# Performance work log

Measured on AMD Instinct MI355X. Metric: run time of the kernel, lower is better.

Reference implementation:

```python
import jax, jax.numpy as jnp
import numpy as np

ROPE_BASE = 10000.0

def _rope(x):
    # x: (B, S, D); canonical interleaved RoPE over sequence positions
    B, S, D = x.shape
    half = D // 2
    inv_freq = 1.0 / (ROPE_BASE ** (jnp.arange(half, dtype=x.dtype) * 2.0 / D))  # (half,)
    ang = jnp.arange(S, dtype=x.dtype)[:, None] * inv_freq[None, :]              # (S, half)
    cos, sin = jnp.cos(ang), jnp.sin(ang)
    x1 = x[..., 0::2]   # (B, S, half)
    x2 = x[..., 1::2]
    rot = jnp.stack([x1 * cos - x2 * sin, x1 * sin + x2 * cos], axis=-1)         # (B,S,half,2)
    return rot.reshape(B, S, D)

def setup_inputs() -> dict:
    key = jax.random.key(0)
    ks = jax.random.split(key, 7)
    B, S, D = 32, 1024, 768
    sc = 1.0 / np.sqrt(D)
    return {
        "x":  jax.random.normal(ks[0], (B, S, D), dtype=jnp.float32),
        "Wq": jax.random.normal(ks[1], (D, D), dtype=jnp.float32) * sc,
        "bq": jax.random.normal(ks[2], (D,), dtype=jnp.float32) * 0.01,
        "Wk": jax.random.normal(ks[3], (D, D), dtype=jnp.float32) * sc,
        "bk": jax.random.normal(ks[4], (D,), dtype=jnp.float32) * 0.01,
        "Wv": jax.random.normal(ks[5], (D, D), dtype=jnp.float32) * sc,
        "bv": jax.random.normal(ks[6], (D,), dtype=jnp.float32) * 0.01,
    }

def reference(x, Wq, bq, Wk, bk, Wv, bv):
    D = x.shape[-1]
    # torch nn.Linear: y = x @ W.T + b
    Q = jnp.einsum('bsd,ed->bse', x, Wq) + bq
    K = jnp.einsum('bsd,ed->bse', x, Wk) + bk
    V = jnp.einsum('bsd,ed->bse', x, Wv) + bv
    Q = _rope(Q)
    K = _rope(K)
    scores = jnp.einsum('bqd,bkd->bqk', Q, K) / jnp.sqrt(jnp.asarray(D, x.dtype))
    weights = jax.nn.softmax(scores, axis=-1)
    return jnp.einsum('bqk,bkd->bqd', weights, V)
```

## Files before the change

### kernel.cpp

```cpp
#include <hip/hip_runtime.h>


typedef __attribute__((ext_vector_type(8))) _Float16 f16x8;
typedef __attribute__((ext_vector_type(4))) float    f32x4;

__device__ __forceinline__ unsigned short f2h(float f) {
    _Float16 h = (_Float16)f;
    return __builtin_bit_cast(unsigned short, h);
}
__device__ __forceinline__ float h2f(unsigned short u) {
    return (float)__builtin_bit_cast(_Float16, u);
}

__device__ __forceinline__ void async_ld16(const void* g, void* l) {
    __builtin_amdgcn_global_load_lds(
        (const __attribute__((address_space(1))) void*)g,
        (__attribute__((address_space(3))) void*)l, 16, 0, 0);
}

template<int MODE, int KDIM, int LDA, int LDB>
__global__ __launch_bounds__(512, 2)
void gemm_bt(const unsigned short* __restrict__ A,
             const unsigned short* __restrict__ B,
             void* __restrict__ C0, void* __restrict__ C1,
             const float* __restrict__ bias0,
             const float* __restrict__ bias1,
             float scale)
{
    __shared__ __align__(16) unsigned short sA[2][256 * 64];
    __shared__ __align__(16) unsigned short sB[2][256 * 64];

    const int tid  = threadIdx.x;
    const int lane = tid & 63;
    const int wave = tid >> 6;
    const int wm   = wave >> 2;
    const int wn   = wave & 3;
    const int wrow = wm * 128;
    const int wcol = wn * 64;
    const int quad = lane >> 4;
    const int l15  = lane & 15;

    const int xcd = blockIdx.x & 7;
    const int bi  = blockIdx.x >> 3;
    int m0, n0, z = 0;
    if constexpr (MODE == 0) {
        m0 = (xcd * 16 + bi / 6) * 256;  n0 = (bi % 6) * 256;
    } else if constexpr (MODE == 1) {
        n0 = (xcd * 16 + bi / 3) * 256;  m0 = (bi % 3) * 256;
    } else if constexpr (MODE == 2) {
        z = xcd * 4 + bi / 16; const int t = bi % 16;
        m0 = (t >> 2) * 256; n0 = (t & 3) * 256;
    } else {
        z = xcd * 4 + bi / 12; const int t = bi % 12;
        m0 = (t / 3) * 256;  n0 = (t % 3) * 256;
    }

    const unsigned short* Ab = A;
    const unsigned short* Bb = B;
    if constexpr (MODE == 2) { Ab += (size_t)z * 786432;  Bb += (size_t)z * 786432; }
    if constexpr (MODE == 3) { Ab += (size_t)z * 1048576; Bb += (size_t)z * 786432; }

    const int srow = tid >> 3;
    const int sk   = ((tid & 7) ^ (srow & 7)) * 8;
    const int sdst = (tid & 7) * 8;

    auto stgA = [&](int buf, int r0, int kt) {
        async_ld16(Ab + (size_t)(m0 + r0 + srow) * LDA + kt + sk,
                   &sA[buf][(r0 + srow) * 64 + sdst]);
    };
    auto stgB = [&](int buf, int r0, int kt) {
        async_ld16(Bb + (size_t)(n0 + r0 + srow) * LDB + kt + sk,
                   &sB[buf][(r0 + srow) * 64 + sdst]);
    };

    f32x4 acc[8][4] = {};

    constexpr int NT = KDIM / 64;

    stgA(0, 0, 0); stgA(0, 128, 0); stgB(0, 0, 0); stgB(0, 64, 0);
    stgA(0, 64, 0); stgA(0, 192, 0); stgB(0, 128, 0); stgB(0, 192, 0);
    stgA(1, 0, 64); stgA(1, 128, 64); stgB(1, 0, 64); stgB(1, 64, 64);
    stgA(1, 64, 64); stgA(1, 192, 64); stgB(1, 128, 64); stgB(1, 192, 64);
    asm volatile("s_waitcnt vmcnt(8)" ::: "memory");
    __builtin_amdgcn_s_barrier();

    int p = 0;
    #pragma unroll 2
    for (int t = 0; t < NT; ++t, p ^= 1) {
        const int  kt2  = (t + 2) * 64;
        const bool pref = (t + 2) < NT;
        const unsigned short* sAp = sA[p];
        const unsigned short* sBp = sB[p];

        f16x8 bfr[4][2], af[4][2];
        #pragma unroll
        for (int ni = 0; ni < 4; ++ni) {
            const int r = wcol + ni * 16 + l15;
            const int x = r & 7;
            bfr[ni][0] = *(const f16x8*)&sBp[r * 64 + ((quad       ^ x) << 3)];
            bfr[ni][1] = *(const f16x8*)&sBp[r * 64 + (((4 + quad) ^ x) << 3)];
        }
        #pragma unroll
        for (int mi = 0; mi < 4; ++mi) {
            const int r = wrow + mi * 16 + l15;
            const int x = r & 7;
            af[mi][0] = *(const f16x8*)&sAp[r * 64 + ((quad       ^ x) << 3)];
            af[mi][1] = *(const f16x8*)&sAp[r * 64 + (((4 + quad) ^ x) << 3)];
        }
        asm volatile("s_waitcnt lgkmcnt(0)" ::: "memory");
        __builtin_amdgcn_s_barrier();
        if (pref) { stgA(p, 0, kt2); stgA(p, 128, kt2);
                    stgB(p, 0, kt2); stgB(p, 64, kt2); }
        __builtin_amdgcn_s_setprio(1);
        #pragma unroll
        for (int mi = 0; mi < 4; ++mi)
            #pragma unroll
            for (int ni = 0; ni < 4; ++ni) {
                acc[mi][ni] = __builtin_amdgcn_mfma_f32_16x16x32_f16(
                    af[mi][0], bfr[ni][0], acc[mi][ni], 0, 0, 0);
                acc[mi][ni] = __builtin_amdgcn_mfma_f32_16x16x32_f16(
                    af[mi][1], bfr[ni][1], acc[mi][ni], 0, 0, 0);
            }
        __builtin_amdgcn_s_setprio(0);

        #pragma unroll
        for (int mi = 0; mi < 4; ++mi) {
            const int r = wrow + 64 + mi * 16 + l15;
            const int x = r & 7;
            af[mi][0] = *(const f16x8*)&sAp[r * 64 + ((quad       ^ x) << 3)];
            af[mi][1] = *(const f16x8*)&sAp[r * 64 + (((4 + quad) ^ x) << 3)];
        }
        asm volatile("s_waitcnt lgkmcnt(0)" ::: "memory");
        __builtin_amdgcn_s_barrier();
        if (pref) { stgA(p, 64, kt2); stgA(p, 192, kt2);
                    stgB(p, 128, kt2); stgB(p, 192, kt2); }
        __builtin_amdgcn_s_setprio(1);
        #pragma unroll
        for (int mi = 0; mi < 4; ++mi)
            #pragma unroll
            for (int ni = 0; ni < 4; ++ni) {
                acc[4 + mi][ni] = __builtin_amdgcn_mfma_f32_16x16x32_f16(
                    af[mi][0], bfr[ni][0], acc[4 + mi][ni], 0, 0, 0);
                acc[4 + mi][ni] = __builtin_amdgcn_mfma_f32_16x16x32_f16(
                    af[mi][1], bfr[ni][1], acc[4 + mi][ni], 0, 0, 0);
            }
        __builtin_amdgcn_s_setprio(0);

        if (pref) asm volatile("s_waitcnt vmcnt(8)" ::: "memory");
        else      asm volatile("s_waitcnt vmcnt(0)" ::: "memory");
        __builtin_amdgcn_s_barrier();
    }

    const bool evenlane = (l15 & 1) == 0;

    float invf[4];
    if constexpr (MODE == 0) {
        #pragma unroll
        for (int ni = 0; ni < 4; ++ni) {
            int col = n0 + wcol + ni * 16 + l15;
            if (col >= 768) col -= 768;
            invf[ni] = exp2f((float)(col >> 1) * -0.03460341765507773f);
        }
    }

    #pragma unroll
    for (int mi = 0; mi < 8; ++mi) {
        const int rowoff = (mi & 3) * 16 + (mi >> 2) * 64;
        #pragma unroll
        for (int ni = 0; ni < 4; ++ni) {
            #pragma unroll
            for (int reg = 0; reg < 4; ++reg) {
                const int grow = m0 + wrow + rowoff + quad * 4 + reg;
                const int gcol = n0 + wcol + ni * 16 + l15;
                float v = acc[mi][ni][reg];
                if constexpr (MODE == 0) {
                    const bool isQ = gcol < 768;
                    const int  col = isQ ? gcol : gcol - 768;
                    v += isQ ? bias0[col] : bias1[col];
                    const float other = __shfl_xor(v, 1);
                    const int   s     = grow & 1023;
                    const float ang   = (float)s * invf[ni];
                    float sn, cs;
                    __sincosf(ang, &sn, &cs);
                    float r = (col & 1) ? fmaf(other, sn, v * cs)
                                        : fmaf(v, cs, -(other * sn));
                    if (isQ) r *= scale;
                    const unsigned short h = f2h(r);
                    const unsigned int packed =
                        (unsigned int)h | (__shfl_xor((unsigned int)h, 1) << 16);
                    if (evenlane) {
                        unsigned short* dst = (unsigned short*)(isQ ? C0 : C1);
                        *(unsigned int*)(dst + (size_t)grow * 768 + col) = packed;
                    }
                } else if constexpr (MODE == 1) {
                    v += bias0[grow];
                    const unsigned short h = f2h(v);
                    const unsigned int packed =
                        (unsigned int)h | (__shfl_xor((unsigned int)h, 1) << 16);
                    if (evenlane) {
                        const int b = gcol >> 10, s = gcol & 1023;
                        *(unsigned int*)((unsigned short*)C0 + (size_t)b * (768 * 1024)
                                         + (size_t)grow * 1024 + s) = packed;
                    }
                } else if constexpr (MODE == 2) {
                    const unsigned short h = f2h(v);
                    const unsigned int packed =
                        (unsigned int)h | (__shfl_xor((unsigned int)h, 1) << 16);
                    if (evenlane) {
                        *(unsigned int*)((unsigned short*)C0 + (size_t)z * 1048576
                                         + (size_t)grow * 1024 + gcol) = packed;
                    }
                } else {
                    const float vo = __shfl_xor(v, 1);
                    if (evenlane) {
                        float2 pk; pk.x = v; pk.y = vo;
                        *(float2*)(((float*)C0) + (size_t)z * 786432
                                   + (size_t)grow * 768 + gcol) = pk;
                    }
                }
            }
        }
    }
}

__global__ __launch_bounds__(256)
void softmax_rows(const unsigned short* __restrict__ S, unsigned short* __restrict__ P)
{
    const int row = blockIdx.x;
    const int tid = threadIdx.x;
    const ushort4 u = ((const ushort4*)(S + (size_t)row * 1024))[tid];
    const float v0 = h2f(u.x), v1 = h2f(u.y), v2 = h2f(u.z), v3 = h2f(u.w);

    float m = fmaxf(fmaxf(v0, v1), fmaxf(v2, v3));
    #pragma unroll
    for (int o = 1; o < 64; o <<= 1) m = fmaxf(m, __shfl_xor(m, o));
    __shared__ float redm[4];
    __shared__ float reds[4];
    const int wave = tid >> 6, lane = tid & 63;
    if (lane == 0) redm[wave] = m;
    __syncthreads();
    m = fmaxf(fmaxf(redm[0], redm[1]), fmaxf(redm[2], redm[3]));

    const float e0 = __expf(v0 - m), e1 = __expf(v1 - m);
    const float e2 = __expf(v2 - m), e3 = __expf(v3 - m);
    float sum = e0 + e1 + e2 + e3;
    #pragma unroll
    for (int o = 1; o < 64; o <<= 1) sum += __shfl_xor(sum, o);
    if (lane == 0) reds[wave] = sum;
    __syncthreads();
    sum = reds[0] + reds[1] + reds[2] + reds[3];
    const float inv = 1.0f / sum;

    ushort4 o4;
    o4.x = f2h(e0 * inv); o4.y = f2h(e1 * inv);
    o4.z = f2h(e2 * inv); o4.w = f2h(e3 * inv);
    ((ushort4*)(P + (size_t)row * 1024))[tid] = o4;
}

__global__ void cvt_f32_f16(const float4* __restrict__ in,
                            ushort4* __restrict__ out, int n4)
{
    int i = blockIdx.x * 256 + threadIdx.x;
    const int stride = gridDim.x * 256;
    for (; i < n4; i += stride) {
        const float4 v = in[i];
        ushort4 o;
        o.x = f2h(v.x); o.y = f2h(v.y); o.z = f2h(v.z); o.w = f2h(v.w);
        out[i] = o;
    }
}

extern "C" void kernel_launch(void* const* d_in, const int* in_sizes, int n_in,
                              void* d_out, int out_size, void* d_ws, size_t ws_size,
                              hipStream_t stream)
{
    const float* x  = (const float*)d_in[0];
    const float* Wq = (const float*)d_in[1];
    const float* bq = (const float*)d_in[2];
    const float* Wk = (const float*)d_in[3];
    const float* bk = (const float*)d_in[4];
    const float* Wv = (const float*)d_in[5];
    const float* bv = (const float*)d_in[6];
    float* out = (float*)d_out;

    char* ws = (char*)d_ws;
    unsigned short* xh  = (unsigned short*)(ws + 0);
    unsigned short* wqk = (unsigned short*)(ws + 50331648);
    unsigned short* wvh = (unsigned short*)(ws + 52690944);
    unsigned short* Qh  = (unsigned short*)(ws + 53870592);
    unsigned short* Kh  = (unsigned short*)(ws + 104202240);
    unsigned short* Vt  = (unsigned short*)(ws + 154533888);
    unsigned short* Sc  = (unsigned short*)(ws + 204865536);
    unsigned short* Ph  = (unsigned short*)(ws + 0);

    cvt_f32_f16<<<4096, 256, 0, stream>>>((const float4*)x,  (ushort4*)xh, 25165824 / 4);
    cvt_f32_f16<<<576,  256, 0, stream>>>((const float4*)Wq, (ushort4*)wqk, 589824 / 4);
    cvt_f32_f16<<<576,  256, 0, stream>>>((const float4*)Wk, (ushort4*)(wqk + 589824), 589824 / 4);
    cvt_f32_f16<<<576,  256, 0, stream>>>((const float4*)Wv, (ushort4*)wvh, 589824 / 4);

    const float qscale = 0.03608439182435161f;

    gemm_bt<0, 768, 768, 768><<<768, 512, 0, stream>>>(
        xh, wqk, Qh, Kh, bq, bk, qscale);
    gemm_bt<1, 768, 768, 768><<<384, 512, 0, stream>>>(
        wvh, xh, Vt, nullptr, bv, nullptr, 1.0f);
    gemm_bt<2, 768, 768, 768><<<512, 512, 0, stream>>>(
        Qh, Kh, Sc, nullptr, nullptr, nullptr, 1.0f);
    softmax_rows<<<32768, 256, 0, stream>>>(Sc, Ph);
    gemm_bt<3, 1024, 1024, 1024><<<384, 512, 0, stream>>>(
        Ph, Vt, out, nullptr, nullptr, nullptr, 1.0f);
}
```

Measured before the change: 521.6 us.

## Restructure GEMM main loop into four-phase ping-pong with staggered A/B prefetch

The K-loop of the fp16 MFMA GEMM is split into four compute phases, each using half of the B fragments, with barriers in between. A tiles are now prefetched one stage ahead into the other buffer and B tiles two stages ahead into the current buffer. The intent is to interleave LDS reads, global-to-LDS async loads and MFMA work more finely and to reduce register pressure from holding all B fragments at once. The cost is extra barriers per iteration and more complex vmcnt accounting, which risks stalls or hazards if the wait counts are wrong.

New measurement: 534.0 us. 1.02x slower.

```diff
diff --git a/kernel.cpp b/kernel.cpp
--- a/kernel.cpp
+++ b/kernel.cpp
@@ -77,29 +77,24 @@
 
     constexpr int NT = KDIM / 64;
 
-    stgA(0, 0, 0); stgA(0, 128, 0); stgB(0, 0, 0); stgB(0, 64, 0);
-    stgA(0, 64, 0); stgA(0, 192, 0); stgB(0, 128, 0); stgB(0, 192, 0);
-    stgA(1, 0, 64); stgA(1, 128, 64); stgB(1, 0, 64); stgB(1, 64, 64);
-    stgA(1, 64, 64); stgA(1, 192, 64); stgB(1, 128, 64); stgB(1, 192, 64);
-    asm volatile("s_waitcnt vmcnt(8)" ::: "memory");
+    stgA(0, 0, 0);   stgA(0, 128, 0);  stgA(0, 64, 0);   stgA(0, 192, 0);
+    stgB(0, 0, 0);   stgB(0, 64, 0);   stgB(0, 128, 0);  stgB(0, 192, 0);
+    stgB(1, 0, 64);  stgB(1, 64, 64);  stgB(1, 128, 64); stgB(1, 192, 64);
+    asm volatile("s_waitcnt vmcnt(4)" ::: "memory");
     __builtin_amdgcn_s_barrier();
 
     int p = 0;
     #pragma unroll 2
     for (int t = 0; t < NT; ++t, p ^= 1) {
-        const int  kt2  = (t + 2) * 64;
-        const bool pref = (t + 2) < NT;
         const unsigned short* sAp = sA[p];
         const unsigned short* sBp = sB[p];
-
-        f16x8 bfr[4][2], af[4][2];
-        #pragma unroll
-        for (int ni = 0; ni < 4; ++ni) {
-            const int r = wcol + ni * 16 + l15;
-            const int x = r & 7;
-            bfr[ni][0] = *(const f16x8*)&sBp[r * 64 + ((quad       ^ x) << 3)];
-            bfr[ni][1] = *(const f16x8*)&sBp[r * 64 + (((4 + quad) ^ x) << 3)];
-        }
+        const int  ktA   = (t + 1) * 64;
+        const int  ktB   = (t + 2) * 64;
+        const bool prefA = (t + 1) < NT;
+        const bool prefB = (t + 2) < NT;
+
+        f16x8 af[4][2], b0[2][2], b1[2][2];
+
         #pragma unroll
         for (int mi = 0; mi < 4; ++mi) {
             const int r = wrow + mi * 16 + l15;
@@ -107,21 +102,51 @@
             af[mi][0] = *(const f16x8*)&sAp[r * 64 + ((quad       ^ x) << 3)];
             af[mi][1] = *(const f16x8*)&sAp[r * 64 + (((4 + quad) ^ x) << 3)];
         }
+        #pragma unroll
+        for (int ni = 0; ni < 2; ++ni) {
+            const int r = wcol + ni * 16 + l15;
+            const int x = r & 7;
+            b0[ni][0] = *(const f16x8*)&sBp[r * 64 + ((quad       ^ x) << 3)];
+            b0[ni][1] = *(const f16x8*)&sBp[r * 64 + (((4 + quad) ^ x) << 3)];
+        }
+        if (prefA) { stgA(p ^ 1, 0, ktA); stgA(p ^ 1, 128, ktA); }
+        __builtin_amdgcn_s_barrier();
         asm volatile("s_waitcnt lgkmcnt(0)" ::: "memory");
-        __builtin_amdgcn_s_barrier();
-        if (pref) { stgA(p, 0, kt2); stgA(p, 128, kt2);
-                    stgB(p, 0, kt2); stgB(p, 64, kt2); }
         __builtin_amdgcn_s_setprio(1);
         #pragma unroll
         for (int mi = 0; mi < 4; ++mi)
             #pragma unroll
-            for (int ni = 0; ni < 4; ++ni) {
+            for (int ni = 0; ni < 2; ++ni) {
                 acc[mi][ni] = __builtin_amdgcn_mfma_f32_16x16x32_f16(
-                    af[mi][0], bfr[ni][0], acc[mi][ni], 0, 0, 0);
+                    af[mi][0], b0[ni][0], acc[mi][ni], 0, 0, 0);
                 acc[mi][ni] = __builtin_amdgcn_mfma_f32_16x16x32_f16(
-                    af[mi][1], bfr[ni][1], acc[mi][ni], 0, 0, 0);
+                    af[mi][1], b0[ni][1], acc[mi][ni], 0, 0, 0);
             }
         __builtin_amdgcn_s_setprio(0);
+        __builtin_amdgcn_s_barrier();
+
+        #pragma unroll
+        for (int ni = 0; ni < 2; ++ni) {
+            const int r = wcol + (2 + ni) * 16 + l15;
+            const int x = r & 7;
+            b1[ni][0] = *(const f16x8*)&sBp[r * 64 + ((quad       ^ x) << 3)];
+            b1[ni][1] = *(const f16x8*)&sBp[r * 64 + (((4 + quad) ^ x) << 3)];
+        }
+        if (prefA) { stgA(p ^ 1, 64, ktA); stgA(p ^ 1, 192, ktA); }
+        __builtin_amdgcn_s_barrier();
+        asm volatile("s_waitcnt lgkmcnt(0)" ::: "memory");
+        __builtin_amdgcn_s_setprio(1);
+        #pragma unroll
+        for (int mi = 0; mi < 4; ++mi)
+            #pragma unroll
+            for (int ni = 0; ni < 2; ++ni) {
+                acc[mi][2 + ni] = __builtin_amdgcn_mfma_f32_16x16x32_f16(
+                    af[mi][0], b1[ni][0], acc[mi][2 + ni], 0, 0, 0);
+                acc[mi][2 + ni] = __builtin_amdgcn_mfma_f32_16x16x32_f16(
+                    af[mi][1], b1[ni][1], acc[mi][2 + ni], 0, 0, 0);
+            }
+        __builtin_amdgcn_s_setprio(0);
+        __builtin_amdgcn_s_barrier();
 
         #pragma unroll
         for (int mi = 0; mi < 4; ++mi) {
@@ -130,25 +155,41 @@
             af[mi][0] = *(const f16x8*)&sAp[r * 64 + ((quad       ^ x) << 3)];
             af[mi][1] = *(const f16x8*)&sAp[r * 64 + (((4 + quad) ^ x) << 3)];
         }
+        if (prefB) { stgB(p, 0, ktB); stgB(p, 64, ktB); }
+        __builtin_amdgcn_s_barrier();
         asm volatile("s_waitcnt lgkmcnt(0)" ::: "memory");
-        __builtin_amdgcn_s_barrier();
-        if (pref) { stgA(p, 64, kt2); stgA(p, 192, kt2);
-                    stgB(p, 128, kt2); stgB(p, 192, kt2); }
         __builtin_amdgcn_s_setprio(1);
         #pragma unroll
         for (int mi = 0; mi < 4; ++mi)
             #pragma unroll
-            for (int ni = 0; ni < 4; ++ni) {
+            for (int ni = 0; ni < 2; ++ni) {
+                acc[4 + mi][2 + ni] = __builtin_amdgcn_mfma_f32_16x16x32_f16(
+                    af[mi][0], b1[ni][0], acc[4 + mi][2 + ni], 0, 0, 0);
+                acc[4 + mi][2 + ni] = __builtin_amdgcn_mfma_f32_16x16x32_f16(
+                    af[mi][1], b1[ni][1], acc[4 + mi][2 + ni], 0, 0, 0);
+            }
+        __builtin_amdgcn_s_setprio(0);
+        __builtin_amdgcn_s_barrier();
+
+        if (prefB) { stgB(p, 128, ktB); stgB(p, 192, ktB); }
+        __builtin_amdgcn_s_setprio(1);
+        #pragma unroll
+        for (int mi = 0; mi < 4; ++mi)
+            #pragma unroll
+            for (int ni = 0; ni < 2; ++ni) {
                 acc[4 + mi][ni] = __builtin_amdgcn_mfma_f32_16x16x32_f16(
-                    af[mi][0], bfr[ni][0], acc[4 + mi][ni], 0, 0, 0);
+                    af[mi][0], b0[ni][0], acc[4 + mi][ni], 0, 0, 0);
                 acc[4 + mi][ni] = __builtin_amdgcn_mfma_f32_16x16x32_f16(
-                    af[mi][1], bfr[ni][1], acc[4 + mi][ni], 0, 0, 0);
+                    af[mi][1], b0[ni][1], acc[4 + mi][ni], 0, 0, 0);
             }
         __builtin_amdgcn_s_setprio(0);
-
-        if (pref) asm volatile("s_waitcnt vmcnt(8)" ::: "memory");
-        else      asm volatile("s_waitcnt vmcnt(0)" ::: "memory");
-        __builtin_amdgcn_s_barrier();
+        if (prefB) {
+            asm volatile("s_waitcnt vmcnt(4)" ::: "memory");
+            __builtin_amdgcn_s_barrier();
+        } else if (prefA) {
+            asm volatile("s_waitcnt vmcnt(0)" ::: "memory");
+            __builtin_amdgcn_s_barrier();
+        }
     }
 
     const bool evenlane = (l15 & 1) == 0;
```

## Replace split two-phase prefetch pipeline with simple one-ahead double buffering

Applied to the files above, without the earlier changes.

Restructures the GEMM main loop. Before, each K-tile was processed in two half-phases with prefetch two tiles ahead. Now the next tile is prefetched once at the start of each step, all 8 A fragments are loaded at once, and the step ends with a full vmcnt(0) wait and a barrier. This cuts the barrier count and simplifies scheduling, but prefetch depth drops to one tile and register pressure rises from holding 16 A fragments, so global-load latency may be exposed more.

Measured after the change: 654.2 us. 25.4% more time.

```diff
diff --git a/kernel.cpp b/kernel.cpp
--- a/kernel.cpp
+++ b/kernel.cpp
@@ -27,8 +27,10 @@
              const float* __restrict__ bias1,
              float scale)
 {
-    __shared__ __align__(16) unsigned short sA[2][256 * 64];
-    __shared__ __align__(16) unsigned short sB[2][256 * 64];
+    __shared__ __align__(16) unsigned short sA0[256 * 64];
+    __shared__ __align__(16) unsigned short sA1[256 * 64];
+    __shared__ __align__(16) unsigned short sB0[256 * 64];
+    __shared__ __align__(16) unsigned short sB1[256 * 64];
 
     const int tid  = threadIdx.x;
     const int lane = tid & 63;
@@ -64,91 +66,68 @@
     const int sk   = ((tid & 7) ^ (srow & 7)) * 8;
     const int sdst = (tid & 7) * 8;
 
-    auto stgA = [&](int buf, int r0, int kt) {
-        async_ld16(Ab + (size_t)(m0 + r0 + srow) * LDA + kt + sk,
-                   &sA[buf][(r0 + srow) * 64 + sdst]);
+    auto stageA = [&](unsigned short* dst, int kt) {
+        #pragma unroll
+        for (int g = 0; g < 4; ++g)
+            async_ld16(Ab + (size_t)(m0 + g * 64 + srow) * LDA + kt + sk,
+                       &dst[(g * 64 + srow) * 64 + sdst]);
     };
-    auto stgB = [&](int buf, int r0, int kt) {
-        async_ld16(Bb + (size_t)(n0 + r0 + srow) * LDB + kt + sk,
-                   &sB[buf][(r0 + srow) * 64 + sdst]);
+    auto stageB = [&](unsigned short* dst, int kt) {
+        #pragma unroll
+        for (int g = 0; g < 4; ++g)
+            async_ld16(Bb + (size_t)(n0 + g * 64 + srow) * LDB + kt + sk,
+                       &dst[(g * 64 + srow) * 64 + sdst]);
     };
 
     f32x4 acc[8][4] = {};
 
     constexpr int NT = KDIM / 64;
 
-    stgA(0, 0, 0); stgA(0, 128, 0); stgB(0, 0, 0); stgB(0, 64, 0);
-    stgA(0, 64, 0); stgA(0, 192, 0); stgB(0, 128, 0); stgB(0, 192, 0);
-    stgA(1, 0, 64); stgA(1, 128, 64); stgB(1, 0, 64); stgB(1, 64, 64);
-    stgA(1, 64, 64); stgA(1, 192, 64); stgB(1, 128, 64); stgB(1, 192, 64);
-    asm volatile("s_waitcnt vmcnt(8)" ::: "memory");
-    __builtin_amdgcn_s_barrier();
-
-    int p = 0;
-    #pragma unroll 2
-    for (int t = 0; t < NT; ++t, p ^= 1) {
-        const int  kt2  = (t + 2) * 64;
-        const bool pref = (t + 2) < NT;
-        const unsigned short* sAp = sA[p];
-        const unsigned short* sBp = sB[p];
-
-        f16x8 bfr[4][2], af[4][2];
+    auto kstep = [&](const unsigned short* Ac, const unsigned short* Bc,
+                     unsigned short* Ao, unsigned short* Bo, int t)
+        __attribute__((always_inline))
+    {
+        if (t + 1 < NT) { stageA(Ao, (t + 1) * 64); stageB(Bo, (t + 1) * 64); }
+
+        f16x8 a[8][2], b[4][2];
         #pragma unroll
         for (int ni = 0; ni < 4; ++ni) {
             const int r = wcol + ni * 16 + l15;
             const int x = r & 7;
-            bfr[ni][0] = *(const f16x8*)&sBp[r * 64 + ((quad       ^ x) << 3)];
-            bfr[ni][1] = *(const f16x8*)&sBp[r * 64 + (((4 + quad) ^ x) << 3)];
-        }
-        #pragma unroll
-        for (int mi = 0; mi < 4; ++mi) {
+            b[ni][0] = *(const f16x8*)&Bc[r * 64 + ((quad       ^ x) << 3)];
+            b[ni][1] = *(const f16x8*)&Bc[r * 64 + (((4 + quad) ^ x) << 3)];
+        }
+        #pragma unroll
+        for (int mi = 0; mi < 8; ++mi) {
             const int r = wrow + mi * 16 + l15;
             const int x = r & 7;
-            af[mi][0] = *(const f16x8*)&sAp[r * 64 + ((quad       ^ x) << 3)];
-            af[mi][1] = *(const f16x8*)&sAp[r * 64 + (((4 + quad) ^ x) << 3)];
-        }
-        asm volatile("s_waitcnt lgkmcnt(0)" ::: "memory");
-        __builtin_amdgcn_s_barrier();
-        if (pref) { stgA(p, 0, kt2); stgA(p, 128, kt2);
-                    stgB(p, 0, kt2); stgB(p, 64, kt2); }
+            a[mi][0] = *(const f16x8*)&Ac[r * 64 + ((quad       ^ x) << 3)];
+            a[mi][1] = *(const f16x8*)&Ac[r * 64 + (((4 + quad) ^ x) << 3)];
+        }
+
         __builtin_amdgcn_s_setprio(1);
         #pragma unroll
-        for (int mi = 0; mi < 4; ++mi)
+        for (int mi = 0; mi < 8; ++mi)
             #pragma unroll
             for (int ni = 0; ni < 4; ++ni) {
                 acc[mi][ni] = __builtin_amdgcn_mfma_f32_16x16x32_f16(
-                    af[mi][0], bfr[ni][0], acc[mi][ni], 0, 0, 0);
+                    a[mi][0], b[ni][0], acc[mi][ni], 0, 0, 0);
                 acc[mi][ni] = __builtin_amdgcn_mfma_f32_16x16x32_f16(
-                    af[mi][1], bfr[ni][1], acc[mi][ni], 0, 0, 0);
+                    a[mi][1], b[ni][1], acc[mi][ni], 0, 0, 0);
             }
         __builtin_amdgcn_s_setprio(0);
 
-        #pragma unroll
-        for (int mi = 0; mi < 4; ++mi) {
-            const int r = wrow + 64 + mi * 16 + l15;
-            const int x = r & 7;
-            af[mi][0] = *(const f16x8*)&sAp[r * 64 + ((quad       ^ x) << 3)];
-            af[mi][1] = *(const f16x8*)&sAp[r * 64 + (((4 + quad) ^ x) << 3)];
-        }
-        asm volatile("s_waitcnt lgkmcnt(0)" ::: "memory");
-        __builtin_amdgcn_s_barrier();
-        if (pref) { stgA(p, 64, kt2); stgA(p, 192, kt2);
-                    stgB(p, 128, kt2); stgB(p, 192, kt2); }
-        __builtin_amdgcn_s_setprio(1);
-        #pragma unroll
-        for (int mi = 0; mi < 4; ++mi)
-            #pragma unroll
-            for (int ni = 0; ni < 4; ++ni) {
-                acc[4 + mi][ni] = __builtin_amdgcn_mfma_f32_16x16x32_f16(
-                    af[mi][0], bfr[ni][0], acc[4 + mi][ni], 0, 0, 0);
-                acc[4 + mi][ni] = __builtin_amdgcn_mfma_f32_16x16x32_f16(
-                    af[mi][1], bfr[ni][1], acc[4 + mi][ni], 0, 0, 0);
-            }
-        __builtin_amdgcn_s_setprio(0);
-
-        if (pref) asm volatile("s_waitcnt vmcnt(8)" ::: "memory");
-        else      asm volatile("s_waitcnt vmcnt(0)" ::: "memory");
-        __builtin_amdgcn_s_barrier();
+        asm volatile("s_waitcnt vmcnt(0)" ::: "memory");
+        asm volatile("s_barrier" ::: "memory");
+    };
+
+    stageA(sA0, 0); stageB(sB0, 0);
+    asm volatile("s_waitcnt vmcnt(0)" ::: "memory");
+    asm volatile("s_barrier" ::: "memory");
+
+    for (int t = 0; t < NT; t += 2) {
+        kstep(sA0, sB0, sA1, sB1, t);
+        kstep(sA1, sB1, sA0, sB0, t + 1);
     }
 
     const bool evenlane = (l15 & 1) == 0;
@@ -165,7 +144,7 @@
 
     #pragma unroll
     for (int mi = 0; mi < 8; ++mi) {
-        const int rowoff = (mi & 3) * 16 + (mi >> 2) * 64;
+        const int rowoff = mi * 16;
         #pragma unroll
         for (int ni = 0; ni < 4; ++ni) {
             #pragma unroll
```
